# Kernel optimization log

Measured on AMD Instinct MI355X. Metric: run time of the kernel, lower is better.

The kernel has to match this reference:

```python
import jax, jax.numpy as jnp
import numpy as np

D_MODEL = 1024
NUM_HEADS = 16
HEAD_DIM = D_MODEL // NUM_HEADS
ROPE_BASE = 10000.0


def _rotate_half(x):
    x1, x2 = jnp.split(x, 2, axis=-1)
    return jnp.concatenate([-x2, x1], axis=-1)


def _rope_cache(seq_len, head_dim, dtype):
    half = head_dim // 2
    inv_freq = 1.0 / (ROPE_BASE ** (jnp.arange(half, dtype=jnp.float32) / float(half)))
    t = jnp.arange(seq_len, dtype=jnp.float32)
    freqs = t[:, None] * inv_freq[None, :]          # [s, half]
    emb = jnp.concatenate([freqs, freqs], axis=-1)   # [s, head_dim]
    cos = jnp.cos(emb)[None, None, :, :].astype(dtype)  # [1,1,s,d]
    sin = jnp.sin(emb)[None, None, :, :].astype(dtype)
    return cos, sin


def setup_inputs() -> dict:
    key = jax.random.key(0)
    k1, k2, k3 = jax.random.split(key, 3)
    b, s = 4, 2048
    x = jax.random.normal(k1, (b, s, D_MODEL), dtype=jnp.float32)
    mask = jnp.ones((b, s), dtype=jnp.float32)
    Wqkv = jax.random.normal(k2, (D_MODEL, 3 * D_MODEL), dtype=jnp.float32) * (D_MODEL ** -0.5)
    Wout = jax.random.normal(k3, (D_MODEL, D_MODEL), dtype=jnp.float32) * (D_MODEL ** -0.5)
    return {"x": x, "mask": mask, "Wqkv": Wqkv, "Wout": Wout}


def reference(x, mask, Wqkv, Wout):
    b, s, _ = x.shape
    qkv = x @ Wqkv                                   # [b,s,3*d_model]
    q, k, v = jnp.split(qkv, 3, axis=-1)

    def split_heads(t):
        return t.reshape(b, s, NUM_HEADS, HEAD_DIM).transpose(0, 2, 1, 3)  # [b,h,s,d]

    q, k, v = map(split_heads, (q, k, v))
    cos, sin = _rope_cache(s, HEAD_DIM, x.dtype)
    q = q * cos + _rotate_half(q) * sin
    k = k * cos + _rotate_half(k) * sin

    scale = HEAD_DIM ** -0.5
    logits = jnp.einsum('bhid,bhjd->bhij', q, k) * scale
    logits = logits + (1.0 - mask)[:, None, None, :] * -1e9
    attn = jax.nn.softmax(logits, axis=-1)
    out = jnp.einsum('bhij,bhjd->bhid', attn, v)     # [b,h,s,d]
    out = out.transpose(0, 2, 1, 3).reshape(b, s, D_MODEL)
    return out @ Wout
```

## Files before the change

kernel.cpp:

```cpp
#include <hip/hip_runtime.h>

typedef unsigned short u16;
typedef unsigned int u32;
typedef int i32x2 __attribute__((ext_vector_type(2)));
typedef float f32x4 __attribute__((ext_vector_type(4)));
typedef float f32x16 __attribute__((ext_vector_type(16)));
typedef __bf16 bf16x8 __attribute__((ext_vector_type(8)));
typedef unsigned short u16x8 __attribute__((ext_vector_type(8)));
typedef unsigned short u16x4 __attribute__((ext_vector_type(4)));
typedef unsigned int u32x4 __attribute__((ext_vector_type(4)));

#define S_ 2048
#define DM 1024

#define LDS_U32(p) ((__attribute__((address_space(3))) unsigned int*)(p))
#define GLB_U32(p) ((const __attribute__((address_space(1))) unsigned int*)(p))

__device__ __forceinline__ u16 f2bf(float f) {
    unsigned int u = __float_as_uint(f);
    u += 0x7fffu + ((u >> 16) & 1u);
    return (u16)(u >> 16);
}
__device__ __forceinline__ float bf2f(u16 s) {
    return __uint_as_float(((unsigned int)s) << 16);
}
__device__ __forceinline__ float fast_exp2(float x) {
#if __has_builtin(__builtin_amdgcn_exp2f)
    return __builtin_amdgcn_exp2f(x);
#else
    return __expf(x * 0.69314718056f);
#endif
}

__global__ __launch_bounds__(256) void f32_to_bf16_kernel(const float* __restrict__ in,
                                                          u16* __restrict__ o, int n) {
    int i = (blockIdx.x * 256 + threadIdx.x) << 2;
    if (i >= n) return;
    float4 f = *(const float4*)&in[i];
    u16x4 r;
    r[0] = f2bf(f.x); r[1] = f2bf(f.y); r[2] = f2bf(f.z); r[3] = f2bf(f.w);
    *(u16x4*)&o[i] = r;
}

__global__ __launch_bounds__(256) void transpose_w(const float* __restrict__ W,
                                                   u16* __restrict__ Wt, int K, int N) {
    __shared__ float tile[32][33];
    int nb = blockIdx.x << 5, kb = blockIdx.y << 5;
    int tx = threadIdx.x & 31, ty = threadIdx.x >> 5;
#pragma unroll
    for (int r = 0; r < 32; r += 8)
        tile[ty + r][tx] = W[(size_t)(kb + ty + r) * N + nb + tx];
    __syncthreads();
#pragma unroll
    for (int r = 0; r < 32; r += 8)
        Wt[(size_t)(nb + ty + r) * K + kb + tx] = f2bf(tile[tx][ty + r]);
}

template <int MODE>
__global__ __launch_bounds__(256) void gemm_bt(const u16* __restrict__ A,
                                               const u16* __restrict__ Bt,
                                               float* __restrict__ Cf,
                                               u16* __restrict__ Qp, u16* __restrict__ Kp,
                                               u16* __restrict__ Vp,
                                               int M, int N, int K) {
    __shared__ __align__(16) u16 Al[128 * 32];
    __shared__ __align__(16) u16 Bl[128 * 32];
    const int tid = threadIdx.x;
    const int Ntiles = N >> 7;
    const int cpx = gridDim.x >> 3;
    const int bid = (int)blockIdx.x;
    const int wg = (bid & 7) * cpx + (bid >> 3);
    const int mt = wg / Ntiles, nt = wg % Ntiles;
    const int m0 = mt << 7, n0 = nt << 7;
    const int wave = tid >> 6, lane = tid & 63;
    const int wm = (wave >> 1) << 6, wn = (wave & 1) << 6;
    const int lr = lane & 15, lk = (lane >> 4) << 3;

    const int srow = (wave << 4) + (lane >> 2);
    const int scol = (lane & 3) << 3;

    f32x4 acc[4][4] = {};

    for (int k0 = 0; k0 < K; k0 += 32) {
        __syncthreads();
#pragma unroll
        for (int i = 0; i < 2; ++i) {
            const u16* ga = &A[(size_t)(m0 + srow + (i << 6)) * K + k0 + scol];
            const u16* gb = &Bt[(size_t)(n0 + srow + (i << 6)) * K + k0 + scol];
            __builtin_amdgcn_global_load_lds(GLB_U32(ga), LDS_U32(&Al[(wave << 9) + (i << 11)]), 16, 0, 0);
            __builtin_amdgcn_global_load_lds(GLB_U32(gb), LDS_U32(&Bl[(wave << 9) + (i << 11)]), 16, 0, 0);
        }
        __syncthreads();
        bf16x8 af[4], bfr[4];
#pragma unroll
        for (int i = 0; i < 4; ++i) {
            af[i]  = __builtin_bit_cast(bf16x8, *(const u16x8*)&Al[(wm + (i << 4) + lr) * 32 + lk]);
            bfr[i] = __builtin_bit_cast(bf16x8, *(const u16x8*)&Bl[(wn + (i << 4) + lr) * 32 + lk]);
        }
#pragma unroll
        for (int i = 0; i < 4; ++i)
#pragma unroll
            for (int j = 0; j < 4; ++j)
                acc[i][j] = __builtin_amdgcn_mfma_f32_16x16x32_bf16(af[i], bfr[j], acc[i][j], 0, 0, 0);
    }

    if (MODE == 0) {
        const int t = (n0 + wn) >> 10;
        if (t < 2) {
            const float LN1E4_32 = 9.210340371976184f / 32.0f;
            const float invf0 = __expf(-(float)lr * LN1E4_32);
            const float invf1 = __expf(-(float)(lr + 16) * LN1E4_32);
#pragma unroll
            for (int i = 0; i < 4; ++i) {
                const int rbase = m0 + wm + (i << 4) + ((lane >> 4) << 2);
#pragma unroll
                for (int jj = 0; jj < 4; ++jj) {
                    const float s = (float)((rbase + jj) & (S_ - 1));
                    float sn0, c0, sn1, c1;
                    __sincosf(s * invf0, &sn0, &c0);
                    __sincosf(s * invf1, &sn1, &c1);
                    const float v0 = acc[i][0][jj], v1 = acc[i][1][jj];
                    const float v2 = acc[i][2][jj], v3 = acc[i][3][jj];
                    acc[i][0][jj] = v0 * c0 - v2 * sn0;
                    acc[i][2][jj] = v2 * c0 + v0 * sn0;
                    acc[i][1][jj] = v1 * c1 - v3 * sn1;
                    acc[i][3][jj] = v3 * c1 + v1 * sn1;
                }
            }
        }
    }

#pragma unroll
    for (int i = 0; i < 4; ++i) {
#pragma unroll
        for (int j = 0; j < 4; ++j) {
            int rbase = m0 + wm + (i << 4) + ((lane >> 4) << 2);
            int col = n0 + wn + (j << 4) + lr;
#pragma unroll
            for (int jj = 0; jj < 4; ++jj) {
                float val = acc[i][j][jj];
                int row = rbase + jj;
                if (MODE == 0) {
                    int t = col >> 10, rem = col & 1023;
                    int h = rem >> 6, d = rem & 63;
                    int b = row >> 11, s = row & 2047;
                    size_t dst = ((size_t)((b << 4) + h) * S_ + s) * 64 + d;
                    u16 bv = f2bf(val);
                    if (t == 0) Qp[dst] = bv;
                    else if (t == 1) Kp[dst] = bv;
                    else Vp[dst] = bv;
                } else {
                    Cf[(size_t)row * N + col] = val;
                }
            }
        }
    }
}

__global__ __launch_bounds__(256) void vtrans_kernel(const u16* __restrict__ v,
                                                     u16* __restrict__ vt) {
    __shared__ __align__(16) u16 t[64][72];
    const int bh = blockIdx.x >> 5, st = blockIdx.x & 31;
    const size_t base = (size_t)bh * (S_ * 64);
    const int s0 = st << 6;
    const int r = threadIdx.x >> 2, c0 = (threadIdx.x & 3) << 4;
    *(u16x8*)&t[r][c0]     = *(const u16x8*)&v[base + (size_t)(s0 + r) * 64 + c0];
    *(u16x8*)&t[r][c0 + 8] = *(const u16x8*)&v[base + (size_t)(s0 + r) * 64 + c0 + 8];
    __syncthreads();
    u16x8 w0, w1;
#pragma unroll
    for (int i = 0; i < 8; ++i) w0[i] = t[c0 + i][r];
#pragma unroll
    for (int i = 0; i < 8; ++i) w1[i] = t[c0 + 8 + i][r];
    *(u16x8*)&vt[base + (size_t)r * S_ + s0 + c0]     = w0;
    *(u16x8*)&vt[base + (size_t)r * S_ + s0 + c0 + 8] = w1;
}

__global__ __launch_bounds__(256, 4) void attn_kernel(const u16* __restrict__ q,
                                                      const u16* __restrict__ k,
                                                      const u16* __restrict__ vt,
                                                      const float* __restrict__ mask,
                                                      u16* __restrict__ outp) {
    __shared__ __align__(16) u16 Kl[2][64 * 64];
    __shared__ __align__(16) u16 Vl[2][64 * 64];
    __shared__ float madd2[2][64];
    __shared__ float bcast[4][32];

    const int tid = threadIdx.x, wave = tid >> 6, lane = tid & 63;
    const int c = lane & 31, hi = lane >> 5, c7 = c & 7;
    const int bh = blockIdx.x & 63, qt = blockIdx.x >> 6;
    const int b = bh >> 4, h = bh & 15;
    const size_t base = (size_t)bh * (S_ * 64);
    const int qrow = (qt << 7) + (wave << 5) + c;

    const float QS = 0.18033688f;

    bf16x8 qf[4];
#pragma unroll
    for (int j = 0; j < 4; ++j) {
        u16x8 raw = *(const u16x8*)&q[base + (size_t)qrow * 64 + j * 16 + hi * 8];
        u16x8 sc;
#pragma unroll
        for (int e = 0; e < 8; ++e) sc[e] = f2bf(bf2f(raw[e]) * QS);
        qf[j] = __builtin_bit_cast(bf16x8, sc);
    }

    f32x16 acc[2] = {};
    float m_run = -1e30f, l_run = 0.f;

    const int sr = tid >> 2, su = (tid & 3) << 1;
    const int so0 = sr * 64 + ((su ^ (sr & 7)) << 3);
    const int so1 = sr * 64 + (((su + 1) ^ (sr & 7)) << 3);

    u16x8 kc0 = *(const u16x8*)&k[base + (size_t)sr * 64 + su * 8];
    u16x8 kc1 = *(const u16x8*)&k[base + (size_t)sr * 64 + su * 8 + 8];
    u16x8 vc0 = *(const u16x8*)&vt[base + (size_t)sr * S_ + su * 8];
    u16x8 vc1 = *(const u16x8*)&vt[base + (size_t)sr * S_ + su * 8 + 8];
    float mval = (tid < 64) ? mask[b * S_ + tid] : 1.0f;

    for (int t = 0; t < 32; ++t) {
        const int bi = t & 1;
        u16* Kb = &Kl[bi][0];
        u16* Vb = &Vl[bi][0];
        *(u16x8*)&Kb[so0] = kc0;
        *(u16x8*)&Kb[so1] = kc1;
        *(u16x8*)&Vb[so0] = vc0;
        *(u16x8*)&Vb[so1] = vc1;
        if (tid < 64) madd2[bi][tid] = (1.0f - mval) * -1.44269504e9f;
        if (t + 1 < 32) {
            const int kn = (t + 1) << 6;
            kc0 = *(const u16x8*)&k[base + (size_t)(kn + sr) * 64 + su * 8];
            kc1 = *(const u16x8*)&k[base + (size_t)(kn + sr) * 64 + su * 8 + 8];
            vc0 = *(const u16x8*)&vt[base + (size_t)sr * S_ + kn + su * 8];
            vc1 = *(const u16x8*)&vt[base + (size_t)sr * S_ + kn + su * 8 + 8];
            mval = (tid < 64) ? mask[b * S_ + kn + tid] : 1.0f;
        }
        __syncthreads();

        f32x16 p[2] = {};
        __builtin_amdgcn_s_setprio(1);
#pragma unroll
        for (int j = 0; j < 4; ++j) {
            const int uo = ((2 * j + hi) ^ c7) << 3;
            bf16x8 ka  = __builtin_bit_cast(bf16x8, *(const u16x8*)&Kb[c * 64 + uo]);
            bf16x8 kb2 = __builtin_bit_cast(bf16x8, *(const u16x8*)&Kb[(32 + c) * 64 + uo]);
            p[0] = __builtin_amdgcn_mfma_f32_32x32x16_bf16(ka,  qf[j], p[0], 0, 0, 0);
            p[1] = __builtin_amdgcn_mfma_f32_32x32x16_bf16(kb2, qf[j], p[1], 0, 0, 0);
        }
        __builtin_amdgcn_s_setprio(0);

        bool hasmask = __any(madd2[bi][lane] != 0.0f);
        if (hasmask) {
#pragma unroll
            for (int tt = 0; tt < 2; ++tt)
#pragma unroll
                for (int rq = 0; rq < 4; ++rq) {
                    float4 mf = *(const float4*)&madd2[bi][tt * 32 + rq * 8 + hi * 4];
                    p[tt][4 * rq + 0] += mf.x;
                    p[tt][4 * rq + 1] += mf.y;
                    p[tt][4 * rq + 2] += mf.z;
                    p[tt][4 * rq + 3] += mf.w;
                }
        }

        float tm[16];
#pragma unroll
        for (int r = 0; r < 16; ++r) tm[r] = fmaxf(p[0][r], p[1][r]);
        float a0 = fmaxf(fmaxf(tm[0], tm[1]), tm[2]);
        float a1 = fmaxf(fmaxf(tm[3], tm[4]), tm[5]);
        float a2 = fmaxf(fmaxf(tm[6], tm[7]), tm[8]);
        float a3 = fmaxf(fmaxf(tm[9], tm[10]), tm[11]);
        float a4 = fmaxf(fmaxf(tm[12], tm[13]), tm[14]);
        float b0 = fmaxf(fmaxf(a0, a1), a2);
        float b1 = fmaxf(fmaxf(a3, a4), tm[15]);
        float mx = fmaxf(b0, b1);
        {
            i32x2 mm = __builtin_amdgcn_permlane32_swap(__float_as_int(mx), __float_as_int(mx), false, false);
            mx = fmaxf(__int_as_float(mm[0]), __int_as_float(mm[1]));
        }

        if (!__all(mx - m_run <= 8.0f)) {
            float mnew = fmaxf(m_run, mx);
            float alpha = fast_exp2(m_run - mnew);
            m_run = mnew;
            l_run *= alpha;
            bcast[wave][c] = alpha;
            float avf[16];
#pragma unroll
            for (int rq = 0; rq < 4; ++rq) {
                float4 t4 = *(const float4*)&bcast[wave][rq * 8 + hi * 4];
                avf[4 * rq + 0] = t4.x; avf[4 * rq + 1] = t4.y;
                avf[4 * rq + 2] = t4.z; avf[4 * rq + 3] = t4.w;
            }
#pragma unroll
            for (int r = 0; r < 16; ++r) {
                acc[0][r] *= avf[r];
                acc[1][r] *= avf[r];
            }
        }

        float s4[4] = {0.f, 0.f, 0.f, 0.f};
#pragma unroll
        for (int tt = 0; tt < 2; ++tt)
#pragma unroll
            for (int r = 0; r < 16; ++r) {
                float e = fast_exp2(p[tt][r] - m_run);
                p[tt][r] = e;
                s4[r & 3] += e;
            }
        float ls = (s4[0] + s4[1]) + (s4[2] + s4[3]);
        {
            i32x2 ss = __builtin_amdgcn_permlane32_swap(__float_as_int(ls), __float_as_int(ls), false, false);
            ls = __int_as_float(ss[0]) + __int_as_float(ss[1]);
        }
        l_run += ls;

        u32 wa[8], wb[8];
#pragma unroll
        for (int tt = 0; tt < 2; ++tt)
#pragma unroll
            for (int rq = 0; rq < 4; ++rq) {
                float e0 = p[tt][4 * rq + 0], e1 = p[tt][4 * rq + 1];
                float e2 = p[tt][4 * rq + 2], e3 = p[tt][4 * rq + 3];
                u32 w0, w1;
                asm("v_cvt_pk_bf16_f32 %0, %1, %2" : "=v"(w0) : "v"(e0), "v"(e1));
                asm("v_cvt_pk_bf16_f32 %0, %1, %2" : "=v"(w1) : "v"(e2), "v"(e3));
                wa[4 * tt + rq] = w0;
                wb[4 * tt + rq] = w1;
            }

        __builtin_amdgcn_s_setprio(1);
#pragma unroll
        for (int ks = 0; ks < 4; ++ks) {
            i32x2 ra = __builtin_amdgcn_permlane32_swap((int)wa[2 * ks], (int)wa[2 * ks + 1], false, false);
            i32x2 rb = __builtin_amdgcn_permlane32_swap((int)wb[2 * ks], (int)wb[2 * ks + 1], false, false);
            u32x4 pw;
            pw[0] = (u32)ra[0];
            pw[1] = (u32)rb[0];
            pw[2] = (u32)ra[1];
            pw[3] = (u32)rb[1];
            bf16x8 paf = __builtin_bit_cast(bf16x8, pw);
            const int uo = ((2 * ks + hi) ^ c7) << 3;
#pragma unroll
            for (int dt = 0; dt < 2; ++dt) {
                bf16x8 vf = __builtin_bit_cast(bf16x8,
                            *(const u16x8*)&Vb[(32 * dt + c) * 64 + uo]);
                acc[dt] = __builtin_amdgcn_mfma_f32_32x32x16_bf16(paf, vf, acc[dt], 0, 0, 0);
            }
        }
        __builtin_amdgcn_s_setprio(0);
    }

    bcast[wave][c] = l_run;
    __builtin_amdgcn_wave_barrier();
    float lvf[16];
#pragma unroll
    for (int rq = 0; rq < 4; ++rq) {
        float4 t4 = *(const float4*)&bcast[wave][rq * 8 + hi * 4];
        lvf[4 * rq + 0] = __builtin_amdgcn_rcpf(t4.x);
        lvf[4 * rq + 1] = __builtin_amdgcn_rcpf(t4.y);
        lvf[4 * rq + 2] = __builtin_amdgcn_rcpf(t4.z);
        lvf[4 * rq + 3] = __builtin_amdgcn_rcpf(t4.w);
    }
    const size_t orow0 = (size_t)b * S_ + (qt << 7) + (wave << 5);
#pragma unroll
    for (int dt = 0; dt < 2; ++dt)
#pragma unroll
        for (int r = 0; r < 16; ++r) {
            int qr = (r & 3) + 8 * (r >> 2) + 4 * hi;
            outp[(orow0 + qr) * DM + h * 64 + dt * 32 + c] = f2bf(acc[dt][r] * lvf[r]);
        }
}

extern "C" void kernel_launch(void* const* d_in, const int* in_sizes, int n_in,
                              void* d_out, int out_size, void* d_ws, size_t ws_size,
                              hipStream_t stream) {
    const float* x    = (const float*)d_in[0];
    const float* mask = (const float*)d_in[1];
    const float* Wqkv = (const float*)d_in[2];
    const float* Wout = (const float*)d_in[3];
    float* out = (float*)d_out;
    char* ws = (char*)d_ws;
    const size_t MB = 1u << 20;
    u16* xb    = (u16*)(ws);
    u16* WqkvT = (u16*)(ws + 16 * MB);
    u16* WoutT = (u16*)(ws + 22 * MB);
    u16* qb    = (u16*)(ws + 24 * MB);
    u16* kb    = (u16*)(ws + 40 * MB);
    u16* vb    = (u16*)(ws + 56 * MB);
    u16* vtb   = xb;
    u16* ao    = vb;

    f32_to_bf16_kernel<<<8192, 256, 0, stream>>>(x, xb, 8192 * 1024);
    transpose_w<<<dim3(96, 32), 256, 0, stream>>>(Wqkv, WqkvT, 1024, 3072);
    transpose_w<<<dim3(32, 32), 256, 0, stream>>>(Wout, WoutT, 1024, 1024);
    gemm_bt<0><<<64 * 24, 256, 0, stream>>>(xb, WqkvT, nullptr, qb, kb, vb, 8192, 3072, 1024);
    vtrans_kernel<<<2048, 256, 0, stream>>>(vb, vtb);
    attn_kernel<<<1024, 256, 0, stream>>>(qb, kb, vtb, mask, ao);
    gemm_bt<1><<<64 * 8, 256, 0, stream>>>(ao, WoutT, out, nullptr, nullptr, nullptr, 8192, 1024, 1024);
}
```

Before: 234.0 us.

## Process two query tiles per wave in attention to reuse K/V LDS loads

Each attention workgroup now handles 256 query rows instead of 128, with every wave owning two 32-row query tiles (A and B) that share the same K and V fragments read from LDS. The grid is halved and launch bounds drop to 2 blocks per SM to leave room for the doubled accumulators. The goal is to halve K/V global and LDS traffic per query and give the scheduler two independent softmax chains to interleave with MFMAs. The cost is higher register pressure, lower occupancy, and fewer blocks (512) to fill the device.

Measured after the change: 223.0 us. -4.7%, faster.

```diff
diff --git a/kernel.cpp b/kernel.cpp
--- a/kernel.cpp
+++ b/kernel.cpp
@@ -176,7 +176,91 @@
     *(u16x8*)&vt[base + (size_t)r * S_ + s0 + c0 + 8] = w1;
 }
 
-__global__ __launch_bounds__(256, 4) void attn_kernel(const u16* __restrict__ q,
+__device__ __forceinline__ void softmax_chain(f32x16* p, f32x16* acc,
+                                              float& m_run, float& l_run,
+                                              u32* wa, u32* wb,
+                                              const float* madd_tile, bool hasmask,
+                                              float* bcast_w, int c, int hi) {
+    if (hasmask) {
+#pragma unroll
+        for (int tt = 0; tt < 2; ++tt)
+#pragma unroll
+            for (int rq = 0; rq < 4; ++rq) {
+                float4 mf = *(const float4*)&madd_tile[tt * 32 + rq * 8 + hi * 4];
+                p[tt][4 * rq + 0] += mf.x;
+                p[tt][4 * rq + 1] += mf.y;
+                p[tt][4 * rq + 2] += mf.z;
+                p[tt][4 * rq + 3] += mf.w;
+            }
+    }
+
+    float tm[16];
+#pragma unroll
+    for (int r = 0; r < 16; ++r) tm[r] = fmaxf(p[0][r], p[1][r]);
+    float a0 = fmaxf(fmaxf(tm[0], tm[1]), tm[2]);
+    float a1 = fmaxf(fmaxf(tm[3], tm[4]), tm[5]);
+    float a2 = fmaxf(fmaxf(tm[6], tm[7]), tm[8]);
+    float a3 = fmaxf(fmaxf(tm[9], tm[10]), tm[11]);
+    float a4 = fmaxf(fmaxf(tm[12], tm[13]), tm[14]);
+    float b0 = fmaxf(fmaxf(a0, a1), a2);
+    float b1 = fmaxf(fmaxf(a3, a4), tm[15]);
+    float mx = fmaxf(b0, b1);
+    {
+        i32x2 mm = __builtin_amdgcn_permlane32_swap(__float_as_int(mx), __float_as_int(mx), false, false);
+        mx = fmaxf(__int_as_float(mm[0]), __int_as_float(mm[1]));
+    }
+
+    if (!__all(mx - m_run <= 8.0f)) {
+        float mnew = fmaxf(m_run, mx);
+        float alpha = fast_exp2(m_run - mnew);
+        m_run = mnew;
+        l_run *= alpha;
+        bcast_w[c] = alpha;
+        float avf[16];
+#pragma unroll
+        for (int rq = 0; rq < 4; ++rq) {
+            float4 t4 = *(const float4*)&bcast_w[rq * 8 + hi * 4];
+            avf[4 * rq + 0] = t4.x; avf[4 * rq + 1] = t4.y;
+            avf[4 * rq + 2] = t4.z; avf[4 * rq + 3] = t4.w;
+        }
+#pragma unroll
+        for (int r = 0; r < 16; ++r) {
+            acc[0][r] *= avf[r];
+            acc[1][r] *= avf[r];
+        }
+    }
+
+    float s4[4] = {0.f, 0.f, 0.f, 0.f};
+#pragma unroll
+    for (int tt = 0; tt < 2; ++tt)
+#pragma unroll
+        for (int r = 0; r < 16; ++r) {
+            float e = fast_exp2(p[tt][r] - m_run);
+            p[tt][r] = e;
+            s4[r & 3] += e;
+        }
+    float ls = (s4[0] + s4[1]) + (s4[2] + s4[3]);
+    {
+        i32x2 ss = __builtin_amdgcn_permlane32_swap(__float_as_int(ls), __float_as_int(ls), false, false);
+        ls = __int_as_float(ss[0]) + __int_as_float(ss[1]);
+    }
+    l_run += ls;
+
+#pragma unroll
+    for (int tt = 0; tt < 2; ++tt)
+#pragma unroll
+        for (int rq = 0; rq < 4; ++rq) {
+            float e0 = p[tt][4 * rq + 0], e1 = p[tt][4 * rq + 1];
+            float e2 = p[tt][4 * rq + 2], e3 = p[tt][4 * rq + 3];
+            u32 w0, w1;
+            asm("v_cvt_pk_bf16_f32 %0, %1, %2" : "=v"(w0) : "v"(e0), "v"(e1));
+            asm("v_cvt_pk_bf16_f32 %0, %1, %2" : "=v"(w1) : "v"(e2), "v"(e3));
+            wa[4 * tt + rq] = w0;
+            wb[4 * tt + rq] = w1;
+        }
+}
+
+__global__ __launch_bounds__(256, 2) void attn_kernel(const u16* __restrict__ q,
                                                       const u16* __restrict__ k,
                                                       const u16* __restrict__ vt,
                                                       const float* __restrict__ mask,
@@ -191,22 +275,29 @@
     const int bh = blockIdx.x & 63, qt = blockIdx.x >> 6;
     const int b = bh >> 4, h = bh & 15;
     const size_t base = (size_t)bh * (S_ * 64);
-    const int qrow = (qt << 7) + (wave << 5) + c;
+    const int qrowA = (qt << 8) + (wave << 5) + c;
+    const int qrowB = qrowA + 128;
 
     const float QS = 0.18033688f;
 
-    bf16x8 qf[4];
+    bf16x8 qfA[4], qfB[4];
 #pragma unroll
     for (int j = 0; j < 4; ++j) {
-        u16x8 raw = *(const u16x8*)&q[base + (size_t)qrow * 64 + j * 16 + hi * 8];
-        u16x8 sc;
-#pragma unroll
-        for (int e = 0; e < 8; ++e) sc[e] = f2bf(bf2f(raw[e]) * QS);
-        qf[j] = __builtin_bit_cast(bf16x8, sc);
-    }
-
-    f32x16 acc[2] = {};
-    float m_run = -1e30f, l_run = 0.f;
+        u16x8 rawA = *(const u16x8*)&q[base + (size_t)qrowA * 64 + j * 16 + hi * 8];
+        u16x8 rawB = *(const u16x8*)&q[base + (size_t)qrowB * 64 + j * 16 + hi * 8];
+        u16x8 scA, scB;
+#pragma unroll
+        for (int e = 0; e < 8; ++e) {
+            scA[e] = f2bf(bf2f(rawA[e]) * QS);
+            scB[e] = f2bf(bf2f(rawB[e]) * QS);
+        }
+        qfA[j] = __builtin_bit_cast(bf16x8, scA);
+        qfB[j] = __builtin_bit_cast(bf16x8, scB);
+    }
+
+    f32x16 accA[2] = {}, accB[2] = {};
+    float m_runA = -1e30f, l_runA = 0.f;
+    float m_runB = -1e30f, l_runB = 0.f;
 
     const int sr = tid >> 2, su = (tid & 3) << 1;
     const int so0 = sr * 64 + ((su ^ (sr & 7)) << 3);
@@ -237,139 +328,93 @@
         }
         __syncthreads();
 
-        f32x16 p[2] = {};
+        f32x16 pA[2] = {}, pB[2] = {};
         __builtin_amdgcn_s_setprio(1);
 #pragma unroll
         for (int j = 0; j < 4; ++j) {
             const int uo = ((2 * j + hi) ^ c7) << 3;
             bf16x8 ka  = __builtin_bit_cast(bf16x8, *(const u16x8*)&Kb[c * 64 + uo]);
             bf16x8 kb2 = __builtin_bit_cast(bf16x8, *(const u16x8*)&Kb[(32 + c) * 64 + uo]);
-            p[0] = __builtin_amdgcn_mfma_f32_32x32x16_bf16(ka,  qf[j], p[0], 0, 0, 0);
-            p[1] = __builtin_amdgcn_mfma_f32_32x32x16_bf16(kb2, qf[j], p[1], 0, 0, 0);
+            pA[0] = __builtin_amdgcn_mfma_f32_32x32x16_bf16(ka,  qfA[j], pA[0], 0, 0, 0);
+            pA[1] = __builtin_amdgcn_mfma_f32_32x32x16_bf16(kb2, qfA[j], pA[1], 0, 0, 0);
+            pB[0] = __builtin_amdgcn_mfma_f32_32x32x16_bf16(ka,  qfB[j], pB[0], 0, 0, 0);
+            pB[1] = __builtin_amdgcn_mfma_f32_32x32x16_bf16(kb2, qfB[j], pB[1], 0, 0, 0);
         }
         __builtin_amdgcn_s_setprio(0);
 
         bool hasmask = __any(madd2[bi][lane] != 0.0f);
-        if (hasmask) {
-#pragma unroll
-            for (int tt = 0; tt < 2; ++tt)
-#pragma unroll
-                for (int rq = 0; rq < 4; ++rq) {
-                    float4 mf = *(const float4*)&madd2[bi][tt * 32 + rq * 8 + hi * 4];
-                    p[tt][4 * rq + 0] += mf.x;
-                    p[tt][4 * rq + 1] += mf.y;
-                    p[tt][4 * rq + 2] += mf.z;
-                    p[tt][4 * rq + 3] += mf.w;
-                }
-        }
-
-        float tm[16];
-#pragma unroll
-        for (int r = 0; r < 16; ++r) tm[r] = fmaxf(p[0][r], p[1][r]);
-        float a0 = fmaxf(fmaxf(tm[0], tm[1]), tm[2]);
-        float a1 = fmaxf(fmaxf(tm[3], tm[4]), tm[5]);
-        float a2 = fmaxf(fmaxf(tm[6], tm[7]), tm[8]);
-        float a3 = fmaxf(fmaxf(tm[9], tm[10]), tm[11]);
-        float a4 = fmaxf(fmaxf(tm[12], tm[13]), tm[14]);
-        float b0 = fmaxf(fmaxf(a0, a1), a2);
-        float b1 = fmaxf(fmaxf(a3, a4), tm[15]);
-        float mx = fmaxf(b0, b1);
-        {
-            i32x2 mm = __builtin_amdgcn_permlane32_swap(__float_as_int(mx), __float_as_int(mx), false, false);
-            mx = fmaxf(__int_as_float(mm[0]), __int_as_float(mm[1]));
-        }
-
-        if (!__all(mx - m_run <= 8.0f)) {
-            float mnew = fmaxf(m_run, mx);
-            float alpha = fast_exp2(m_run - mnew);
-            m_run = mnew;
-            l_run *= alpha;
-            bcast[wave][c] = alpha;
-            float avf[16];
-#pragma unroll
-            for (int rq = 0; rq < 4; ++rq) {
-                float4 t4 = *(const float4*)&bcast[wave][rq * 8 + hi * 4];
-                avf[4 * rq + 0] = t4.x; avf[4 * rq + 1] = t4.y;
-                avf[4 * rq + 2] = t4.z; avf[4 * rq + 3] = t4.w;
-            }
-#pragma unroll
-            for (int r = 0; r < 16; ++r) {
-                acc[0][r] *= avf[r];
-                acc[1][r] *= avf[r];
-            }
-        }
-
-        float s4[4] = {0.f, 0.f, 0.f, 0.f};
-#pragma unroll
-        for (int tt = 0; tt < 2; ++tt)
-#pragma unroll
-            for (int r = 0; r < 16; ++r) {
-                float e = fast_exp2(p[tt][r] - m_run);
-                p[tt][r] = e;
-                s4[r & 3] += e;
-            }
-        float ls = (s4[0] + s4[1]) + (s4[2] + s4[3]);
-        {
-            i32x2 ss = __builtin_amdgcn_permlane32_swap(__float_as_int(ls), __float_as_int(ls), false, false);
-            ls = __int_as_float(ss[0]) + __int_as_float(ss[1]);
-        }
-        l_run += ls;
-
-        u32 wa[8], wb[8];
-#pragma unroll
-        for (int tt = 0; tt < 2; ++tt)
-#pragma unroll
-            for (int rq = 0; rq < 4; ++rq) {
-                float e0 = p[tt][4 * rq + 0], e1 = p[tt][4 * rq + 1];
-                float e2 = p[tt][4 * rq + 2], e3 = p[tt][4 * rq + 3];
-                u32 w0, w1;
-                asm("v_cvt_pk_bf16_f32 %0, %1, %2" : "=v"(w0) : "v"(e0), "v"(e1));
-                asm("v_cvt_pk_bf16_f32 %0, %1, %2" : "=v"(w1) : "v"(e2), "v"(e3));
-                wa[4 * tt + rq] = w0;
-                wb[4 * tt + rq] = w1;
-            }
+
+        u32 waA[8], wbA[8], waB[8], wbB[8];
+        softmax_chain(pA, accA, m_runA, l_runA, waA, wbA, &madd2[bi][0], hasmask, &bcast[wave][0], c, hi);
+        softmax_chain(pB, accB, m_runB, l_runB, waB, wbB, &madd2[bi][0], hasmask, &bcast[wave][0], c, hi);
 
         __builtin_amdgcn_s_setprio(1);
 #pragma unroll
         for (int ks = 0; ks < 4; ++ks) {
-            i32x2 ra = __builtin_amdgcn_permlane32_swap((int)wa[2 * ks], (int)wa[2 * ks + 1], false, false);
-            i32x2 rb = __builtin_amdgcn_permlane32_swap((int)wb[2 * ks], (int)wb[2 * ks + 1], false, false);
-            u32x4 pw;
-            pw[0] = (u32)ra[0];
-            pw[1] = (u32)rb[0];
-            pw[2] = (u32)ra[1];
-            pw[3] = (u32)rb[1];
-            bf16x8 paf = __builtin_bit_cast(bf16x8, pw);
+            i32x2 raA = __builtin_amdgcn_permlane32_swap((int)waA[2 * ks], (int)waA[2 * ks + 1], false, false);
+            i32x2 rbA = __builtin_amdgcn_permlane32_swap((int)wbA[2 * ks], (int)wbA[2 * ks + 1], false, false);
+            i32x2 raB = __builtin_amdgcn_permlane32_swap((int)waB[2 * ks], (int)waB[2 * ks + 1], false, false);
+            i32x2 rbB = __builtin_amdgcn_permlane32_swap((int)wbB[2 * ks], (int)wbB[2 * ks + 1], false, false);
+            u32x4 pwA, pwB;
+            pwA[0] = (u32)raA[0]; pwA[1] = (u32)rbA[0]; pwA[2] = (u32)raA[1]; pwA[3] = (u32)rbA[1];
+            pwB[0] = (u32)raB[0]; pwB[1] = (u32)rbB[0]; pwB[2] = (u32)raB[1]; pwB[3] = (u32)rbB[1];
+            bf16x8 pafA = __builtin_bit_cast(bf16x8, pwA);
+            bf16x8 pafB = __builtin_bit_cast(bf16x8, pwB);
             const int uo = ((2 * ks + hi) ^ c7) << 3;
 #pragma unroll
             for (int dt = 0; dt < 2; ++dt) {
                 bf16x8 vf = __builtin_bit_cast(bf16x8,
                             *(const u16x8*)&Vb[(32 * dt + c) * 64 + uo]);
-                acc[dt] = __builtin_amdgcn_mfma_f32_32x32x16_bf16(paf, vf, acc[dt], 0, 0, 0);
+                accA[dt] = __builtin_amdgcn_mfma_f32_32x32x16_bf16(pafA, vf, accA[dt], 0, 0, 0);
+                accB[dt] = __builtin_amdgcn_mfma_f32_32x32x16_bf16(pafB, vf, accB[dt], 0, 0, 0);
             }
         }
         __builtin_amdgcn_s_setprio(0);
     }
 
-    bcast[wave][c] = l_run;
-    __builtin_amdgcn_wave_barrier();
-    float lvf[16];
-#pragma unroll
-    for (int rq = 0; rq < 4; ++rq) {
-        float4 t4 = *(const float4*)&bcast[wave][rq * 8 + hi * 4];
-        lvf[4 * rq + 0] = __builtin_amdgcn_rcpf(t4.x);
-        lvf[4 * rq + 1] = __builtin_amdgcn_rcpf(t4.y);
-        lvf[4 * rq + 2] = __builtin_amdgcn_rcpf(t4.z);
-        lvf[4 * rq + 3] = __builtin_amdgcn_rcpf(t4.w);
-    }
-    const size_t orow0 = (size_t)b * S_ + (qt << 7) + (wave << 5);
-#pragma unroll
-    for (int dt = 0; dt < 2; ++dt)
-#pragma unroll
-        for (int r = 0; r < 16; ++r) {
-            int qr = (r & 3) + 8 * (r >> 2) + 4 * hi;
-            outp[(orow0 + qr) * DM + h * 64 + dt * 32 + c] = f2bf(acc[dt][r] * lvf[r]);
-        }
+    {
+        bcast[wave][c] = l_runA;
+        __builtin_amdgcn_wave_barrier();
+        float lvf[16];
+#pragma unroll
+        for (int rq = 0; rq < 4; ++rq) {
+            float4 t4 = *(const float4*)&bcast[wave][rq * 8 + hi * 4];
+            lvf[4 * rq + 0] = __builtin_amdgcn_rcpf(t4.x);
+            lvf[4 * rq + 1] = __builtin_amdgcn_rcpf(t4.y);
+            lvf[4 * rq + 2] = __builtin_amdgcn_rcpf(t4.z);
+            lvf[4 * rq + 3] = __builtin_amdgcn_rcpf(t4.w);
+        }
+        const size_t orow0 = (size_t)b * S_ + (qt << 8) + (wave << 5);
+#pragma unroll
+        for (int dt = 0; dt < 2; ++dt)
+#pragma unroll
+            for (int r = 0; r < 16; ++r) {
+                int qr = (r & 3) + 8 * (r >> 2) + 4 * hi;
+                outp[(orow0 + qr) * DM + h * 64 + dt * 32 + c] = f2bf(accA[dt][r] * lvf[r]);
+            }
+    }
+    {
+        __builtin_amdgcn_wave_barrier();
+        bcast[wave][c] = l_runB;
+        __builtin_amdgcn_wave_barrier();
+        float lvf[16];
+#pragma unroll
+        for (int rq = 0; rq < 4; ++rq) {
+            float4 t4 = *(const float4*)&bcast[wave][rq * 8 + hi * 4];
+            lvf[4 * rq + 0] = __builtin_amdgcn_rcpf(t4.x);
+            lvf[4 * rq + 1] = __builtin_amdgcn_rcpf(t4.y);
+            lvf[4 * rq + 2] = __builtin_amdgcn_rcpf(t4.z);
+            lvf[4 * rq + 3] = __builtin_amdgcn_rcpf(t4.w);
+        }
+        const size_t orow0 = (size_t)b * S_ + (qt << 8) + (wave << 5) + 128;
+#pragma unroll
+        for (int dt = 0; dt < 2; ++dt)
+#pragma unroll
+            for (int r = 0; r < 16; ++r) {
+                int qr = (r & 3) + 8 * (r >> 2) + 4 * hi;
+                outp[(orow0 + qr) * DM + h * 64 + dt * 32 + c] = f2bf(accB[dt][r] * lvf[r]);
+            }
+    }
 }
 
 extern "C" void kernel_launch(void* const* d_in, const int* in_sizes, int n_in,
@@ -396,6 +441,6 @@
     transpose_w<<<dim3(32, 32), 256, 0, stream>>>(Wout, WoutT, 1024, 1024);
     gemm_bt<0><<<64 * 24, 256, 0, stream>>>(xb, WqkvT, nullptr, qb, kb, vb, 8192, 3072, 1024);
     vtrans_kernel<<<2048, 256, 0, stream>>>(vb, vtb);
-    attn_kernel<<<1024, 256, 0, stream>>>(qb, kb, vtb, mask, ao);
+    attn_kernel<<<512, 256, 0, stream>>>(qb, kb, vtb, mask, ao);
     gemm_bt<1><<<64 * 8, 256, 0, stream>>>(ao, WoutT, out, nullptr, nullptr, nullptr, 8192, 1024, 1024);
 }
```
